# Kernel tuning notes

Measured on AMD Instinct MI355X. Metric: run time of the kernel, lower is better.

The kernel has to match this reference:

```python
import jax, jax.numpy as jnp
import numpy as np

B, L, C, H, W = 1, 16, 16, 128, 256  # L = T_chunk = K_chunk (single chunk, causal)
DECAY = 0.1  # decay_val


def setup_inputs() -> dict:
    key = jax.random.key(0)
    k1, k2 = jax.random.split(key)
    img = jax.random.normal(k1, (B, L, C, H, W), jnp.float32)
    # flows in normalized [-1,1] grid units; keep displacements modest
    cum_flow = jax.random.normal(k2, (B, L, 2, H, W), jnp.float32) * 0.1
    t = jnp.arange(L)
    mask = (t[:, None] >= t[None, :]).astype(jnp.float32)          # causal [T,K]
    decay_dist = jnp.abs(t[:, None] - t[None, :]).astype(jnp.float32)  # [T,K]
    return {"img": img, "cum_flow": cum_flow, "mask": mask, "decay_dist": decay_dist}


def _bilinear_sample(img, gx, gy):
    # img: [B,K,C,H,W]; gx, gy: [B,K,H,W] in normalized [-1,1] coords.
    # x wraps around (periodic), y clamps -- matching the kernel's index handling.
    ix = (gx + 1.0) * (W * 0.5) - 0.5
    iy = (gy + 1.0) * (H * 0.5) - 0.5
    x0 = jnp.floor(ix)
    y0 = jnp.floor(iy)
    wx = ix - x0  # fractional weights
    wy = iy - y0
    x0i = x0.astype(jnp.int32)
    y0i = y0.astype(jnp.int32)
    x0r = jnp.mod(x0i, W)
    x1r = jnpp = jnp.mod(x0i + 1, W)
    y0c = jnp.clip(y0i, 0, H - 1)
    y1c = jnp.clip(y0i + 1, 0, H - 1)

    K = img.shape[1]
    imgf = img.reshape(B, K, C, H * W)

    def gather(yy, xx):
        idx = (yy * W + xx).reshape(B, K, 1, H * W)  # broadcast over C
        return jnp.take_along_axis(imgf, idx, axis=-1).reshape(B, K, C, H, W)

    va = gather(y0c, x0r)  # (y0, x0)
    vb = gather(y1c, x0r)  # (y1, x0)
    vc = gather(y0c, x1r)  # (y0, x1)
    vd = gather(y1c, x1r)  # (y1, x1)
    wx_ = wx[:, :, None]   # [B,K,1,H,W]
    wy_ = wy[:, :, None]
    return (va * (1.0 - wx_) * (1.0 - wy_) + vb * (1.0 - wx_) * wy_
            + vc * wx_ * (1.0 - wy_) + vd * wx_ * wy_)


def reference(img, cum_flow, mask, decay_dist):
    # base grid (align_corners=False style pixel centers)
    base_x = (jnp.arange(W, dtype=jnp.float32) * (2.0 / W) - 1.0 + 1.0 / W)[None, None, :]  # [1,1,W]
    base_y = (jnp.arange(H, dtype=jnp.float32) * (2.0 / H) - 1.0 + 1.0 / H)[None, :, None]  # [1,H,1]

    weights = mask * jnp.exp(-DECAY * decay_dist)  # [T,K] decay-weighted causal mask
    fx = cum_flow[:, :, 0]  # [B,L,H,W]
    fy = cum_flow[:, :, 1]

    def step(carry, inp):
        ft_x, ft_y, w_row = inp  # ft_*: [B,H,W]; w_row: [K]
        gx = base_x[None] + (ft_x[:, None] - fx)  # [B,K,H,W]
        gy = base_y[None] + (ft_y[:, None] - fy)
        gx = jnp.mod(gx + 1.0, 2.0) - 1.0          # wrap x into [-1,1)
        sampled = _bilinear_sample(img, gx, gy)    # [B,K,C,H,W]
        out_t = jnp.einsum('k,bkchw->bchw', w_row, sampled)
        return carry, out_t

    xs = (jnp.moveaxis(fx, 1, 0), jnp.moveaxis(fy, 1, 0), weights)  # over t
    _, outs = jax.lax.scan(step, 0.0, xs)          # [T,B,C,H,W]
    return jnp.moveaxis(outs, 0, 1)                # [B,T,C,H,W]
```

## Files before the change

kernel.cpp:

```cpp
#include <hip/hip_runtime.h>
#include <hip/hip_fp16.h>

constexpr int Lc = 16;
constexpr int Cc = 16;
constexpr int Hc = 128;
constexpr int Wc = 256;
constexpr float DECAYc = 0.1f;
constexpr int HWc = Hc * Wc;

__global__ __launch_bounds__(256) void transpose_cvt_f16(
    const float* __restrict__ img, __half* __restrict__ imgTh)
{
    const int tid = threadIdx.x;
    const int h2 = tid & 1;
    const int wq = tid >> 1;
    const int kf  = blockIdx.x >> 5;
    const int px0 = (blockIdx.x & 31) * 1024;
    const float* __restrict__ srcb =
        img + (size_t)kf * Cc * HWc + (size_t)(8 * h2) * HWc;
#pragma unroll
    for (int rr = 0; rr < 8; ++rr) {
        const int px = px0 + rr * 128 + wq;
        float v[8];
#pragma unroll
        for (int c = 0; c < 8; ++c) v[c] = srcb[c * HWc + px];
        __half2 h[4];
#pragma unroll
        for (int i = 0; i < 4; ++i)
            h[i] = __float22half2_rn(make_float2(v[2 * i], v[2 * i + 1]));
        *(uint4*)(imgTh + ((size_t)kf * HWc + px) * Cc + 8 * h2) = *(uint4*)h;
    }
}

template <int I0>
__device__ __forceinline__ void chunk4p(
    int k, int p, const __half* __restrict__ bkq,
    const float* sx1, const float* sy1, float fxk, float fyk,
    const float* e2, float epk, float4* acc)
{
    uint2 ld [4][4];
    float wts[4][4];
    int  offs[4][4];

#pragma unroll
    for (int j = 0; j < 4; ++j) {
        const int i = I0 + j;
        const int t = 2 * i + p;
        if (t > k) {
            const float wkt = e2[i] * epk;

            float a = sx1[i] - fxk;
            a -= 2.0f * floorf(a * 0.5f);
            const float X  = a * (Wc * 0.5f) + 255.5f;
            const float Xf = floorf(X);
            const float wx = X - Xf;
            const int xp  = (int)Xf;
            const int x0r = xp & (Wc - 1);
            const int x1r = (xp + 1) & (Wc - 1);

            const float iy = (sy1[i] - fyk) * (Hc * 0.5f) - 0.5f;
            const float Yf = floorf(iy);
            const float wy = iy - Yf;
            const int y0  = (int)Yf;
            const int y0c = min(max(y0, 0), Hc - 1);
            const int y1c = min(max(y0 + 1, 0), Hc - 1);

            const float wb = wkt * wy;
            const float wa = wkt - wb;
            const float omx = 1.0f - wx;
            wts[j][0] = wa * omx;
            wts[j][1] = wa * wx;
            wts[j][2] = wb * omx;
            wts[j][3] = wb * wx;

            const int r0 = y0c << 8, r1 = y1c << 8;
            offs[j][0] = r0 | x0r;
            offs[j][1] = r0 | x1r;
            offs[j][2] = r1 | x0r;
            offs[j][3] = r1 | x1r;
        }
    }
#pragma unroll
    for (int j = 0; j < 4; ++j) {
        const int t = 2 * (I0 + j) + p;
        if (t > k) {
#pragma unroll
            for (int n = 0; n < 4; ++n)
                ld[j][n] = *(const uint2*)(bkq + (size_t)offs[j][n] * Cc);
        }
    }
#pragma unroll
    for (int j = 0; j < 4; ++j) {
        const int i = I0 + j;
        const int t = 2 * i + p;
        if (t > k) {
#pragma unroll
            for (int n = 0; n < 4; ++n) {
                const __half2* hp = (const __half2*)&ld[j][n];
                const float a = wts[j][n];
                acc[i].x += a * __half2float(__low2half (hp[0]));
                acc[i].y += a * __half2float(__high2half(hp[0]));
                acc[i].z += a * __half2float(__low2half (hp[1]));
                acc[i].w += a * __half2float(__high2half(hp[1]));
            }
        }
    }
}

__global__ __launch_bounds__(256, 4) void gridsample_f16_par(
    const __half* __restrict__ imgTh,
    const float* __restrict__ cum_flow,
    const float* __restrict__ img,
    float* __restrict__ out)
{
    const int tid = threadIdx.x;
    const int q  = tid & 3;
    const int wq = tid >> 2;
    const int b = blockIdx.x;
    const int band = b & 7;
    const int p    = (b >> 3) & 1;
    const int sub  = b >> 4;
    const int h = band * 16 + (sub >> 2);
    const int w = (sub & 3) * 64 + wq;
    const int pix = h * Wc + w;

    const float base_x = w * (2.0f / Wc) - 1.0f + 1.0f / Wc;
    const float base_y = h * (2.0f / Hc) - 1.0f + 1.0f / Hc;

    float sx1[8], sy1[8], e2[8];
#pragma unroll
    for (int i = 0; i < 8; ++i) {
        const int t = 2 * i + p;
        sx1[i] = base_x + cum_flow[(t * 2 + 0) * HWc + pix] + 1.0f;
        sy1[i] = base_y + cum_flow[(t * 2 + 1) * HWc + pix] + 1.0f;
        e2[i]  = __expf(-2.0f * DECAYc * (float)i);
    }

    float4 acc[8];
#pragma unroll
    for (int i = 0; i < 8; ++i) acc[i] = make_float4(0.f, 0.f, 0.f, 0.f);

    float epk = p ? 0.9048374180359595f : 1.0f;
    const int kmax = 13 + p;
    for (int k = 0; k <= kmax; ++k) {
        const float fxk = cum_flow[(k * 2 + 0) * HWc + pix];
        const float fyk = cum_flow[(k * 2 + 1) * HWc + pix];
        const __half* __restrict__ bkq = imgTh + (size_t)k * HWc * Cc + 4 * q;

        chunk4p<0>(k, p, bkq, sx1, sy1, fxk, fyk, e2, epk, acc);
        chunk4p<4>(k, p, bkq, sx1, sy1, fxk, fyk, e2, epk, acc);

        epk *= 1.1051709180756477f;
    }

#pragma unroll
    for (int i = 0; i < 8; ++i) {
        const int t = 2 * i + p;
        const float* __restrict__ ip = img + ((size_t)t * Cc + 4 * q) * HWc + pix;
        float* __restrict__ op = out + ((size_t)t * Cc + 4 * q) * HWc + pix;
        op[0 * HWc] = acc[i].x + ip[0 * HWc];
        op[1 * HWc] = acc[i].y + ip[1 * HWc];
        op[2 * HWc] = acc[i].z + ip[2 * HWc];
        op[3 * HWc] = acc[i].w + ip[3 * HWc];
    }
}

__global__ __launch_bounds__(256) void gridsample_warp_acc(
    const float* __restrict__ img, const float* __restrict__ cum_flow,
    const float* __restrict__ mask, const float* __restrict__ decay,
    float* __restrict__ out)
{
    const int w = threadIdx.x, h = blockIdx.x, t = blockIdx.y;
    const int pix = h * Wc + w;
    const float base_x = w * (2.0f / Wc) - 1.0f + 1.0f / Wc;
    const float base_y = h * (2.0f / Hc) - 1.0f + 1.0f / Hc;
    const float fxt = cum_flow[(t * 2 + 0) * HWc + pix];
    const float fyt = cum_flow[(t * 2 + 1) * HWc + pix];
    float acc[Cc];
#pragma unroll
    for (int c = 0; c < Cc; ++c) acc[c] = 0.0f;
    for (int k = 0; k <= t; ++k) {
        const float wkt = mask[t * Lc + k] * __expf(-DECAYc * decay[t * Lc + k]);
        const float fxk = cum_flow[(k * 2 + 0) * HWc + pix];
        const float fyk = cum_flow[(k * 2 + 1) * HWc + pix];
        float gx = base_x + (fxt - fxk);
        const float gy = base_y + (fyt - fyk);
        float m = gx + 1.0f;
        m -= 2.0f * floorf(m * 0.5f);
        gx = m - 1.0f;
        const float ix = (gx + 1.0f) * (Wc * 0.5f) - 0.5f;
        const float iy = (gy + 1.0f) * (Hc * 0.5f) - 0.5f;
        const float x0f = floorf(ix), y0f = floorf(iy);
        const float wx = ix - x0f, wy = iy - y0f;
        const int x0 = (int)x0f, y0 = (int)y0f;
        const int x0r = x0 & (Wc - 1), x1r = (x0 + 1) & (Wc - 1);
        const int y0c = min(max(y0, 0), Hc - 1), y1c = min(max(y0 + 1, 0), Hc - 1);
        const float a00 = wkt * (1.0f - wx) * (1.0f - wy);
        const float a01 = wkt * (1.0f - wx) * wy;
        const float a10 = wkt * wx * (1.0f - wy);
        const float a11 = wkt * wx * wy;
        const int o00 = y0c * Wc + x0r, o01 = y1c * Wc + x0r;
        const int o10 = y0c * Wc + x1r, o11 = y1c * Wc + x1r;
        const float* __restrict__ ik = img + (size_t)k * Cc * HWc;
#pragma unroll
        for (int c = 0; c < Cc; ++c) {
            const float* __restrict__ p = ik + c * HWc;
            acc[c] += p[o00] * a00 + p[o01] * a01 + p[o10] * a10 + p[o11] * a11;
        }
    }
    float* __restrict__ op = out + (size_t)t * Cc * HWc + pix;
#pragma unroll
    for (int c = 0; c < Cc; ++c) op[c * HWc] = acc[c];
}

extern "C" void kernel_launch(void* const* d_in, const int* in_sizes, int n_in,
                              void* d_out, int out_size, void* d_ws, size_t ws_size,
                              hipStream_t stream) {
    const float* img      = (const float*)d_in[0];
    const float* cum_flow = (const float*)d_in[1];
    const float* mask     = (const float*)d_in[2];
    const float* decay    = (const float*)d_in[3];
    float* out = (float*)d_out;

    const size_t needed = (size_t)Lc * HWc * Cc * sizeof(__half);
    if (ws_size >= needed) {
        __half* imgTh = (__half*)d_ws;
        transpose_cvt_f16<<<dim3(512), 256, 0, stream>>>(img, imgTh);
        gridsample_f16_par<<<dim3(1024), 256, 0, stream>>>(
            imgTh, cum_flow, img, out);
    } else {
        dim3 grid(Hc, Lc, 1);
        gridsample_warp_acc<<<grid, Wc, 0, stream>>>(img, cum_flow, mask, decay, out);
    }
}
```

Baseline: 151.5 us.

## Pad image rows with wrap column so each lane loads an x-pair with one wide load

New measurement: 223.6 us. 47.5% more time.

```diff
diff --git a/kernel.cpp b/kernel.cpp
--- a/kernel.cpp
+++ b/kernel.cpp
@@ -5,22 +5,27 @@
 constexpr int Cc = 16;
 constexpr int Hc = 128;
 constexpr int Wc = 256;
+constexpr int WP = 257;
 constexpr float DECAYc = 0.1f;
 constexpr int HWc = Hc * Wc;
-
-__global__ __launch_bounds__(256) void transpose_cvt_f16(
+constexpr int RSh = WP * Cc;
+constexpr int FRh = Hc * RSh;
+
+__global__ __launch_bounds__(256) void transpose_cvt_f16p(
     const float* __restrict__ img, __half* __restrict__ imgTh)
 {
     const int tid = threadIdx.x;
     const int h2 = tid & 1;
     const int wq = tid >> 1;
-    const int kf  = blockIdx.x >> 5;
-    const int px0 = (blockIdx.x & 31) * 1024;
+    const int kf  = blockIdx.x >> 6;
+    const int px0 = (blockIdx.x & 63) * 512;
     const float* __restrict__ srcb =
         img + (size_t)kf * Cc * HWc + (size_t)(8 * h2) * HWc;
 #pragma unroll
-    for (int rr = 0; rr < 8; ++rr) {
+    for (int rr = 0; rr < 4; ++rr) {
         const int px = px0 + rr * 128 + wq;
+        const int y = px >> 8;
+        const int x = px & 255;
         float v[8];
 #pragma unroll
         for (int c = 0; c < 8; ++c) v[c] = srcb[c * HWc + px];
@@ -28,19 +33,24 @@
 #pragma unroll
         for (int i = 0; i < 4; ++i)
             h[i] = __float22half2_rn(make_float2(v[2 * i], v[2 * i + 1]));
-        *(uint4*)(imgTh + ((size_t)kf * HWc + px) * Cc + 8 * h2) = *(uint4*)h;
+        __half* __restrict__ dst =
+            imgTh + (size_t)kf * FRh + (size_t)y * RSh + x * Cc + 8 * h2;
+        *(uint4*)dst = *(uint4*)h;
+        if (x == 0)
+            *(uint4*)(dst + 256 * Cc) = *(uint4*)h;
     }
 }
 
 template <int I0>
-__device__ __forceinline__ void chunk4p(
-    int k, int p, const __half* __restrict__ bkq,
+__device__ __forceinline__ void chunk4x(
+    int k, int p, const __half* __restrict__ bq,
+    float wxsel,
     const float* sx1, const float* sy1, float fxk, float fyk,
-    const float* e2, float epk, float4* acc)
-{
-    uint2 ld [4][4];
-    float wts[4][4];
-    int  offs[4][4];
+    const float* e2, float epk, float4 (*acc2)[2])
+{
+    uint4 ld [4][2];
+    float wts[4][2];
+    int  offs[4][2];
 
 #pragma unroll
     for (int j = 0; j < 4; ++j) {
@@ -56,7 +66,6 @@
             const float wx = X - Xf;
             const int xp  = (int)Xf;
             const int x0r = xp & (Wc - 1);
-            const int x1r = (xp + 1) & (Wc - 1);
 
             const float iy = (sy1[i] - fyk) * (Hc * 0.5f) - 0.5f;
             const float Yf = floorf(iy);
@@ -65,28 +74,22 @@
             const int y0c = min(max(y0, 0), Hc - 1);
             const int y1c = min(max(y0 + 1, 0), Hc - 1);
 
-            const float wb = wkt * wy;
-            const float wa = wkt - wb;
-            const float omx = 1.0f - wx;
-            wts[j][0] = wa * omx;
-            wts[j][1] = wa * wx;
-            wts[j][2] = wb * omx;
-            wts[j][3] = wb * wx;
-
-            const int r0 = y0c << 8, r1 = y1c << 8;
-            offs[j][0] = r0 | x0r;
-            offs[j][1] = r0 | x1r;
-            offs[j][2] = r1 | x0r;
-            offs[j][3] = r1 | x1r;
+            const float wxs = wxsel ? wx : (1.0f - wx);
+            const float wyb = wkt * wy;
+            wts[j][0] = (wkt - wyb) * wxs;
+            wts[j][1] = wyb * wxs;
+
+            const int xo = x0r * Cc;
+            offs[j][0] = y0c * RSh + xo;
+            offs[j][1] = y1c * RSh + xo;
         }
     }
 #pragma unroll
     for (int j = 0; j < 4; ++j) {
         const int t = 2 * (I0 + j) + p;
         if (t > k) {
-#pragma unroll
-            for (int n = 0; n < 4; ++n)
-                ld[j][n] = *(const uint2*)(bkq + (size_t)offs[j][n] * Cc);
+            ld[j][0] = *(const uint4*)(bq + offs[j][0]);
+            ld[j][1] = *(const uint4*)(bq + offs[j][1]);
         }
     }
 #pragma unroll
@@ -95,19 +98,23 @@
         const int t = 2 * i + p;
         if (t > k) {
 #pragma unroll
-            for (int n = 0; n < 4; ++n) {
-                const __half2* hp = (const __half2*)&ld[j][n];
-                const float a = wts[j][n];
-                acc[i].x += a * __half2float(__low2half (hp[0]));
-                acc[i].y += a * __half2float(__high2half(hp[0]));
-                acc[i].z += a * __half2float(__low2half (hp[1]));
-                acc[i].w += a * __half2float(__high2half(hp[1]));
+            for (int r = 0; r < 2; ++r) {
+                const __half2* hp = (const __half2*)&ld[j][r];
+                const float a = wts[j][r];
+                acc2[i][0].x += a * __half2float(__low2half (hp[0]));
+                acc2[i][0].y += a * __half2float(__high2half(hp[0]));
+                acc2[i][0].z += a * __half2float(__low2half (hp[1]));
+                acc2[i][0].w += a * __half2float(__high2half(hp[1]));
+                acc2[i][1].x += a * __half2float(__low2half (hp[2]));
+                acc2[i][1].y += a * __half2float(__high2half(hp[2]));
+                acc2[i][1].z += a * __half2float(__low2half (hp[3]));
+                acc2[i][1].w += a * __half2float(__high2half(hp[3]));
             }
         }
     }
 }
 
-__global__ __launch_bounds__(256, 4) void gridsample_f16_par(
+__global__ __launch_bounds__(256, 4) void gridsample_f16_xpair(
     const __half* __restrict__ imgTh,
     const float* __restrict__ cum_flow,
     const float* __restrict__ img,
@@ -115,6 +122,8 @@
 {
     const int tid = threadIdx.x;
     const int q  = tid & 3;
+    const int xs = q >> 1;
+    const int hf = q & 1;
     const int wq = tid >> 2;
     const int b = blockIdx.x;
     const int band = b & 7;
@@ -136,32 +145,45 @@
         e2[i]  = __expf(-2.0f * DECAYc * (float)i);
     }
 
-    float4 acc[8];
-#pragma unroll
-    for (int i = 0; i < 8; ++i) acc[i] = make_float4(0.f, 0.f, 0.f, 0.f);
-
+    float4 acc2[8][2];
+#pragma unroll
+    for (int i = 0; i < 8; ++i) {
+        acc2[i][0] = make_float4(0.f, 0.f, 0.f, 0.f);
+        acc2[i][1] = make_float4(0.f, 0.f, 0.f, 0.f);
+    }
+
+    const float wxsel = (float)xs;
     float epk = p ? 0.9048374180359595f : 1.0f;
     const int kmax = 13 + p;
     for (int k = 0; k <= kmax; ++k) {
         const float fxk = cum_flow[(k * 2 + 0) * HWc + pix];
         const float fyk = cum_flow[(k * 2 + 1) * HWc + pix];
-        const __half* __restrict__ bkq = imgTh + (size_t)k * HWc * Cc + 4 * q;
-
-        chunk4p<0>(k, p, bkq, sx1, sy1, fxk, fyk, e2, epk, acc);
-        chunk4p<4>(k, p, bkq, sx1, sy1, fxk, fyk, e2, epk, acc);
+        const __half* __restrict__ bq = imgTh + (size_t)k * FRh + 8 * q;
+
+        chunk4x<0>(k, p, bq, wxsel, sx1, sy1, fxk, fyk, e2, epk, acc2);
+        chunk4x<4>(k, p, bq, wxsel, sx1, sy1, fxk, fyk, e2, epk, acc2);
 
         epk *= 1.1051709180756477f;
     }
 
+    const int cpl = hf * 8 + xs * 4;
 #pragma unroll
     for (int i = 0; i < 8; ++i) {
         const int t = 2 * i + p;
-        const float* __restrict__ ip = img + ((size_t)t * Cc + 4 * q) * HWc + pix;
-        float* __restrict__ op = out + ((size_t)t * Cc + 4 * q) * HWc + pix;
-        op[0 * HWc] = acc[i].x + ip[0 * HWc];
-        op[1 * HWc] = acc[i].y + ip[1 * HWc];
-        op[2 * HWc] = acc[i].z + ip[2 * HWc];
-        op[3 * HWc] = acc[i].w + ip[3 * HWc];
+#pragma unroll
+        for (int d = 0; d < 2; ++d) {
+            acc2[i][d].x += __shfl_xor(acc2[i][d].x, 2);
+            acc2[i][d].y += __shfl_xor(acc2[i][d].y, 2);
+            acc2[i][d].z += __shfl_xor(acc2[i][d].z, 2);
+            acc2[i][d].w += __shfl_xor(acc2[i][d].w, 2);
+        }
+        const float4 s = acc2[i][xs];
+        const float* __restrict__ ip = img + ((size_t)t * Cc + cpl) * HWc + pix;
+        float* __restrict__ op = out + ((size_t)t * Cc + cpl) * HWc + pix;
+        op[0 * HWc] = s.x + ip[0 * HWc];
+        op[1 * HWc] = s.y + ip[1 * HWc];
+        op[2 * HWc] = s.z + ip[2 * HWc];
+        op[3 * HWc] = s.w + ip[3 * HWc];
     }
 }
 
@@ -222,11 +244,11 @@
     const float* decay    = (const float*)d_in[3];
     float* out = (float*)d_out;
 
-    const size_t needed = (size_t)Lc * HWc * Cc * sizeof(__half);
+    const size_t needed = (size_t)Lc * FRh * sizeof(__half);
     if (ws_size >= needed) {
         __half* imgTh = (__half*)d_ws;
-        transpose_cvt_f16<<<dim3(512), 256, 0, stream>>>(img, imgTh);
-        gridsample_f16_par<<<dim3(1024), 256, 0, stream>>>(
+        transpose_cvt_f16p<<<dim3(1024), 256, 0, stream>>>(img, imgTh);
+        gridsample_f16_xpair<<<dim3(1024), 256, 0, stream>>>(
             imgTh, cum_flow, img, out);
     } else {
         dim3 grid(Hc, Lc, 1);
```
